# Performance work log

Measured on AMD Instinct MI355X. Metric: run time of the kernel, lower is better.

## Reference

```python
import jax, jax.numpy as jnp
import numpy as np

B, C, H, W = 32, 3, 512, 512


def _make_rot(N):
    k = np.arange(N, dtype=np.float64)[None, :] * np.pi / (2 * N)
    return jnp.asarray(np.cos(k), jnp.float32), jnp.asarray(np.sin(k), jnp.float32)


def setup_inputs() -> dict:
    key = jax.random.key(0)
    X = jax.random.normal(key, (B, C, H, W), dtype=jnp.float32)
    W_r_weight, W_i_weight = _make_rot(W)
    W_r_height, W_i_height = _make_rot(H)
    return {
        "X": X,
        "W_r_weight": W_r_weight,
        "W_i_weight": W_i_weight,
        "W_r_height": W_r_height,
        "W_i_height": W_i_height,
    }


def _idct1(X, W_r, W_i):
    # 1D IDCT (DCT-III) along last axis via irfft, norm='ortho'.
    shp = X.shape
    N = shp[-1]
    Xv = X.reshape(-1, N) * 0.5
    # ortho scaling: col 0 -> *sqrt(N)*2, cols 1: -> *sqrt(N/2)*2 (after the /2)
    col_scale = np.full((N,), np.sqrt(N / 2) * 2, dtype=np.float32)
    col_scale[0] = np.sqrt(N) * 2
    Xv = Xv * jnp.asarray(col_scale)
    # V_t_i[:, 0] = 0; V_t_i[:, j] = -Xv[:, N-j] for j >= 1
    Vti = jnp.concatenate([jnp.zeros_like(Xv[:, :1]), -Xv[:, :0:-1]], axis=1)
    Vr = Xv * W_r - Vti * W_i
    Vi = Xv * W_i + Vti * W_r
    v = jnp.fft.irfft(jax.lax.complex(Vr, Vi), n=N, axis=1)  # [M, N] real
    # de-interleave: even outputs from front half, odd outputs from reversed tail
    x = jnp.zeros_like(v)
    x = x.at[:, ::2].set(v[:, : N - N // 2])
    x = x.at[:, 1::2].set(v[:, ::-1][:, : N // 2])
    return x.reshape(shp)


def reference(X, W_r_weight, W_i_weight, W_r_height, W_i_height):
    x = _idct1(X, W_r_weight, W_i_weight)          # IDCT over width
    x = jnp.swapaxes(x, -1, -2)
    x = _idct1(x, W_r_height, W_i_height)          # IDCT over height
    return jnp.swapaxes(x, -1, -2)
```

## Files before the change

### kernel.cpp

```cpp
#include <hip/hip_runtime.h>
#include <math.h>
#include <stdint.h>

#define N512 512

typedef __attribute__((ext_vector_type(8))) short short8;
typedef __attribute__((ext_vector_type(4))) float floatx4;

#define VMCNT(n) asm volatile("s_waitcnt vmcnt(" #n ")" ::: "memory")
#define LGKM0    asm volatile("s_waitcnt lgkmcnt(0)" ::: "memory")
#define FENCE    asm volatile("" ::: "memory")
#define BARRIER  __builtin_amdgcn_s_barrier()

__device__ __forceinline__ short f2bf(float f) {
    uint32_t u = __float_as_uint(f);
    uint32_t r = u + 0x7fffu + ((u >> 16) & 1u);
    return (short)(r >> 16);
}

__device__ __forceinline__ short f2bf_fast(float f) {
    return (short)((__float_as_uint(f) + 0x8000u) >> 16);
}

__device__ __forceinline__ void gload_lds16(const void* g, void* l) {
    __builtin_amdgcn_global_load_lds(
        (const __attribute__((address_space(1))) void*)g,
        (__attribute__((address_space(3))) void*)l,
        16, 0, 0);
}

__global__ __launch_bounds__(256) void build_idct_matrix_bf16(short* __restrict__ M) {
    int idx = blockIdx.x * 256 + threadIdx.x;
    int n = idx >> 9;
    int k = idx & 511;
    int j = (k * (2 * n + 1)) & (4 * N512 - 1);
    float theta = (float)j * (3.14159265358979323846f / (2.0f * (float)N512));
    float s = (k == 0) ? 0.044194173824159216f : 0.0625f;
    M[idx] = f2bf(s * cosf(theta));
}

__global__ __launch_bounds__(256) void gemm_s1(const short* __restrict__ A,
                                               const float* __restrict__ Xg,
                                               short* __restrict__ Tg) {
    __shared__ __align__(16) short lds[4 * 8192];

    const int t = threadIdx.x;
    const int w = t >> 6;
    const int l = t & 63;
    const int q = (t >> 4) & 3;
    const int r = t & 15;

    const int bm0 = blockIdx.y * 128;
    const int bn0 = blockIdx.x * 128;
    const int wm0 = (w >> 1) * 64;
    const int wn0 = (w & 1) * 64;

    const float* Xs = Xg + ((long)blockIdx.z << 18);
    short* Tt = Tg + ((long)blockIdx.z << 18);

    const int rsub = l >> 3;
    const int glog = (l & 7) ^ rsub;

    const int brow = t >> 4;
    const int col4 = t & 15;
    const int bg   = col4 >> 1;
    const int bh   = col4 & 1;

    floatx4 acc[4][4] = {};
    float4 v[8];

#pragma unroll
    for (int p = 0; p < 8; ++p) {
        const int rt = p * 16 + brow;
        v[p] = *(const float4*)(Xs + (((long)(bn0 + rt)) << 9) + col4 * 4);
    }
#pragma unroll
    for (int i = 0; i < 4; ++i) {
        const int chunk = w * 4 + i;
        const int rt = chunk * 8 + rsub;
        gload_lds16(A + (((long)(bm0 + rt)) << 9) + glog * 8,
                    lds + chunk * 512);
    }
    VMCNT(4);
#pragma unroll
    for (int p = 0; p < 8; ++p) {
        const int rt = p * 16 + brow;
        const int bchunk = rt >> 3;
        const int brs = rt & 7;
        short4 o;
        o.x = f2bf_fast(v[p].x);
        o.y = f2bf_fast(v[p].y);
        o.z = f2bf_fast(v[p].z);
        o.w = f2bf_fast(v[p].w);
        *(short4*)(lds + 8192 + bchunk * 512 + brs * 64 + ((bg ^ brs) * 8) + bh * 4) = o;
    }
    LGKM0;

    for (int kt = 0; kt < 8; ++kt) {
        short* bufc = lds + (kt & 1) * 16384;
        short* bufn = lds + ((kt + 1) & 1) * 16384;

        if (kt < 7) {
            const int k0n = (kt + 1) * 64;
#pragma unroll
            for (int p = 0; p < 8; ++p) {
                const int rt = p * 16 + brow;
                v[p] = *(const float4*)(Xs + (((long)(bn0 + rt)) << 9) + k0n + col4 * 4);
            }
#pragma unroll
            for (int i = 0; i < 4; ++i) {
                const int chunk = w * 4 + i;
                const int rt = chunk * 8 + rsub;
                gload_lds16(A + (((long)(bm0 + rt)) << 9) + k0n + glog * 8,
                            bufn + chunk * 512);
            }
            VMCNT(12);
        } else {
            VMCNT(0);
        }
        BARRIER;
        FENCE;

        {
            short* ldsA = bufc;
            short* ldsB = bufc + 8192;
#pragma unroll
            for (int kk = 0; kk < 2; ++kk) {
                const int c = kk * 4 + q;
                const int goff = ((c ^ (r & 7)) * 8);
                short8 af[4], bfr[4];
#pragma unroll
                for (int i = 0; i < 4; ++i) {
                    af[i]  = *(const short8*)(ldsA + (wm0 + i * 16 + r) * 64 + goff);
                    bfr[i] = *(const short8*)(ldsB + (wn0 + i * 16 + r) * 64 + goff);
                }
#pragma unroll
                for (int i = 0; i < 4; ++i)
#pragma unroll
                    for (int j = 0; j < 4; ++j)
                        acc[i][j] = __builtin_amdgcn_mfma_f32_16x16x32_bf16(
                            af[i], bfr[j], acc[i][j], 0, 0, 0);
            }
        }

        FENCE;
        BARRIER;

        if (kt < 7) {
            VMCNT(4);
#pragma unroll
            for (int p = 0; p < 8; ++p) {
                const int rt = p * 16 + brow;
                const int bchunk = rt >> 3;
                const int brs = rt & 7;
                short4 o;
                o.x = f2bf_fast(v[p].x);
                o.y = f2bf_fast(v[p].y);
                o.z = f2bf_fast(v[p].z);
                o.w = f2bf_fast(v[p].w);
                *(short4*)(bufn + 8192 + bchunk * 512 + brs * 64 + ((bg ^ brs) * 8) + bh * 4) = o;
            }
            LGKM0;
        }
    }

#pragma unroll
    for (int i = 0; i < 4; ++i) {
        const int mrow = bm0 + wm0 + i * 16 + q * 4;
#pragma unroll
        for (int j = 0; j < 4; ++j) {
            const int ncol = bn0 + wn0 + j * 16 + r;
#pragma unroll
            for (int rg = 0; rg < 4; ++rg)
                Tt[(long)(mrow + rg) * N512 + ncol] = f2bf(acc[i][j][rg]);
        }
    }
}

__global__ __launch_bounds__(256) void gemm_s2(const short* __restrict__ A,
                                               const short* __restrict__ Bg,
                                               float* __restrict__ Cg) {
    __shared__ __align__(16) short lds[4 * 8192];

    const int t = threadIdx.x;
    const int w = t >> 6;
    const int l = t & 63;
    const int q = (t >> 4) & 3;
    const int r = t & 15;

    const int bm0 = blockIdx.y * 128;
    const int bn0 = blockIdx.x * 128;
    const int wm0 = (w >> 1) * 64;
    const int wn0 = (w & 1) * 64;

    const short* Bs = Bg + ((long)blockIdx.z << 18);
    float* C = Cg + ((long)blockIdx.z << 18);

    const int rsub = l >> 3;
    const int glog = (l & 7) ^ rsub;

    floatx4 acc[4][4] = {};

#pragma unroll
    for (int i = 0; i < 4; ++i) {
        const int chunk = w * 4 + i;
        const int rt = chunk * 8 + rsub;
        gload_lds16(A + (((long)(bm0 + rt)) << 9) + glog * 8,
                    lds + chunk * 512);
        gload_lds16(Bs + (((long)(bn0 + rt)) << 9) + glog * 8,
                    lds + 8192 + chunk * 512);
    }

    for (int kt = 0; kt < 8; ++kt) {
        short* bufc = lds + (kt & 1) * 16384;
        short* bufn = lds + ((kt + 1) & 1) * 16384;

        if (kt < 7) {
            const int k0n = (kt + 1) * 64;
#pragma unroll
            for (int i = 0; i < 4; ++i) {
                const int chunk = w * 4 + i;
                const int rt = chunk * 8 + rsub;
                gload_lds16(A + (((long)(bm0 + rt)) << 9) + k0n + glog * 8,
                            bufn + chunk * 512);
                gload_lds16(Bs + (((long)(bn0 + rt)) << 9) + k0n + glog * 8,
                            bufn + 8192 + chunk * 512);
            }
            VMCNT(8);
        } else {
            VMCNT(0);
        }
        BARRIER;
        FENCE;

        {
            short* ldsA = bufc;
            short* ldsB = bufc + 8192;
#pragma unroll
            for (int kk = 0; kk < 2; ++kk) {
                const int c = kk * 4 + q;
                const int goff = ((c ^ (r & 7)) * 8);
                short8 af[4], bfr[4];
#pragma unroll
                for (int i = 0; i < 4; ++i) {
                    af[i]  = *(const short8*)(ldsA + (wm0 + i * 16 + r) * 64 + goff);
                    bfr[i] = *(const short8*)(ldsB + (wn0 + i * 16 + r) * 64 + goff);
                }
#pragma unroll
                for (int i = 0; i < 4; ++i)
#pragma unroll
                    for (int j = 0; j < 4; ++j)
                        acc[i][j] = __builtin_amdgcn_mfma_f32_16x16x32_bf16(
                            af[i], bfr[j], acc[i][j], 0, 0, 0);
            }
        }

        FENCE;
        BARRIER;
    }

#pragma unroll
    for (int i = 0; i < 4; ++i) {
        const int mrow = bm0 + wm0 + i * 16 + q * 4;
#pragma unroll
        for (int j = 0; j < 4; ++j) {
            const int ncol = bn0 + wn0 + j * 16 + r;
#pragma unroll
            for (int rg = 0; rg < 4; ++rg)
                C[(long)(mrow + rg) * N512 + ncol] = acc[i][j][rg];
        }
    }
}

extern "C" void kernel_launch(void* const* d_in, const int* in_sizes, int n_in,
                              void* d_out, int out_size, void* d_ws, size_t ws_size,
                              hipStream_t stream) {
    const float* X = (const float*)d_in[0];
    float* out = (float*)d_out;

    const long plane = (long)N512 * N512;
    const int slices = in_sizes[0] / (int)plane;

    short* Mb = (short*)d_ws;
    short* Tt = Mb + plane;

    long avail = (long)ws_size - plane * 2;
    int chunk = (int)(avail / (plane * 2));
    if (chunk > slices) chunk = slices;
    if (chunk >= 32) chunk &= ~31;
    if (chunk < 1) chunk = 1;

    build_idct_matrix_bf16<<<dim3((int)(plane / 256)), dim3(256), 0, stream>>>(Mb);

    for (int s0 = 0; s0 < slices; s0 += chunk) {
        int c = (s0 + chunk <= slices) ? chunk : (slices - s0);
        gemm_s1<<<dim3(4, 4, c), dim3(256), 0, stream>>>(
            Mb, X + (long)s0 * plane, Tt);
        gemm_s2<<<dim3(4, 4, c), dim3(256), 0, stream>>>(
            Mb, Tt, out + (long)s0 * plane);
    }
}
```

Before: 232.4 us.

## Swizzle gemm_s1 block order and stage output through LDS for coalesced stores

Launches gemm_s1 on a flattened 1D grid and decodes block indices so that consecutive workgroups pair slices and their tiles, aiming at better cache locality across the machine's dies or XCDs. The epilogue first writes the bf16 accumulators into padded LDS, then issues 16-byte row-contiguous global stores, replacing the scattered 2-byte stores. The chunk size is also rounded to an even count so the swizzle's assumption holds. The LDS staging adds a barrier and reuses the main LDS buffer for the epilogue.

```diff
diff --git a/kernel.cpp b/kernel.cpp
--- a/kernel.cpp
+++ b/kernel.cpp
@@ -27,6 +27,17 @@
         (const __attribute__((address_space(1))) void*)g,
         (__attribute__((address_space(3))) void*)l,
         16, 0, 0);
+}
+
+__device__ __forceinline__ void decode_swz(int L, int nz,
+                                           int& bx, int& by, int& bz) {
+    if (nz & 1) {
+        bx = L & 3; by = (L >> 2) & 3; bz = L >> 4;
+    } else {
+        const int g = L >> 5, s = L & 31;
+        const int u = (g << 3) | (s & 7);
+        by = s >> 3; bx = u & 3; bz = u >> 2;
+    }
 }
 
 __global__ __launch_bounds__(256) void build_idct_matrix_bf16(short* __restrict__ M) {
@@ -50,13 +61,16 @@
     const int q = (t >> 4) & 3;
     const int r = t & 15;
 
-    const int bm0 = blockIdx.y * 128;
-    const int bn0 = blockIdx.x * 128;
+    int bx, by, bz;
+    decode_swz(blockIdx.x, (int)gridDim.x >> 4, bx, by, bz);
+
+    const int bm0 = by * 128;
+    const int bn0 = bx * 128;
     const int wm0 = (w >> 1) * 64;
     const int wn0 = (w & 1) * 64;
 
-    const float* Xs = Xg + ((long)blockIdx.z << 18);
-    short* Tt = Tg + ((long)blockIdx.z << 18);
+    const float* Xs = Xg + ((long)bz << 18);
+    short* Tt = Tg + ((long)bz << 18);
 
     const int rsub = l >> 3;
     const int glog = (l & 7) ^ rsub;
@@ -164,15 +178,27 @@
         }
     }
 
-#pragma unroll
-    for (int i = 0; i < 4; ++i) {
-        const int mrow = bm0 + wm0 + i * 16 + q * 4;
-#pragma unroll
-        for (int j = 0; j < 4; ++j) {
-            const int ncol = bn0 + wn0 + j * 16 + r;
-#pragma unroll
-            for (int rg = 0; rg < 4; ++rg)
-                Tt[(long)(mrow + rg) * N512 + ncol] = f2bf(acc[i][j][rg]);
+    {
+        short* cst = lds;
+#pragma unroll
+        for (int i = 0; i < 4; ++i) {
+            const int rl = wm0 + i * 16 + q * 4;
+#pragma unroll
+            for (int j = 0; j < 4; ++j) {
+                const int cl = wn0 + j * 16 + r;
+#pragma unroll
+                for (int rg = 0; rg < 4; ++rg)
+                    cst[(rl + rg) * 132 + cl] = f2bf(acc[i][j][rg]);
+            }
+        }
+        __syncthreads();
+        const int orow = t >> 4;
+        const int ocol = (t & 15) * 8;
+#pragma unroll
+        for (int it = 0; it < 8; ++it) {
+            const int rr = it * 16 + orow;
+            short8 vv = *(const short8*)(cst + rr * 132 + ocol);
+            *(short8*)(Tt + (long)(bm0 + rr) * N512 + bn0 + ocol) = vv;
         }
     }
 }
@@ -288,13 +314,14 @@
     int chunk = (int)(avail / (plane * 2));
     if (chunk > slices) chunk = slices;
     if (chunk >= 32) chunk &= ~31;
+    else if (chunk >= 2) chunk &= ~1;
     if (chunk < 1) chunk = 1;
 
     build_idct_matrix_bf16<<<dim3((int)(plane / 256)), dim3(256), 0, stream>>>(Mb);
 
     for (int s0 = 0; s0 < slices; s0 += chunk) {
         int c = (s0 + chunk <= slices) ? chunk : (slices - s0);
-        gemm_s1<<<dim3(4, 4, c), dim3(256), 0, stream>>>(
+        gemm_s1<<<dim3(16 * c), dim3(256), 0, stream>>>(
             Mb, X + (long)s0 * plane, Tt);
         gemm_s2<<<dim3(4, 4, c), dim3(256), 0, stream>>>(
             Mb, Tt, out + (long)s0 * plane);
```

Measured after the change: 230.7 us. No clear change (-0.7%).
